# Performance work log

Hardware: AMD Instinct MI355X
Metric: run time of the kernel (lower is better)

Reference implementation:

```python
import jax, jax.numpy as jnp
import numpy as np


def gcn_conv(x, W, b, src, dst, num_nodes):
    """PyG GCNConv with add_self_loops=True, symmetric normalization, bias.
    src/dst already include self-loops. deg computed from unit edge weights."""
    deg = jax.ops.segment_sum(jnp.ones(src.shape[0], x.dtype), dst,
                              num_segments=num_nodes)
    dinv = jnp.where(deg > 0, jax.lax.rsqrt(deg), 0.0)
    norm = dinv[src] * dinv[dst]               # [E]
    h = x @ W                                  # [N, F_out] dense GEMM first
    msg = h[src] * norm[:, None]               # gather + scale, [E, F_out]
    out = jax.ops.segment_sum(msg, dst, num_segments=num_nodes)  # scatter-add
    return out + b


def setup_inputs() -> dict:
    key = jax.random.key(0)
    ks = jax.random.split(key, 5)
    N, E, F_in, F_out = 50000, 800000, 512, 40
    x = jax.random.normal(ks[0], (N, F_in), dtype=jnp.float32)
    edge_index = jax.random.randint(ks[1], (2, E), 0, N, dtype=jnp.int64)
    W1 = jax.random.normal(ks[2], (F_in, 256), dtype=jnp.float32) * (F_in ** -0.5)
    W2 = jax.random.normal(ks[3], (256, 16), dtype=jnp.float32) * (256 ** -0.5)
    W3 = jax.random.normal(ks[4], (16, F_out), dtype=jnp.float32) * (16 ** -0.5)
    return {
        "x": x, "edge_index": edge_index,
        "W1": W1, "b1": jnp.zeros((256,), jnp.float32),
        "W2": W2, "b2": jnp.zeros((16,), jnp.float32),
        "W3": W3, "b3": jnp.zeros((F_out,), jnp.float32),
    }


def reference(x, edge_index, W1, b1, W2, b2, W3, b3):
    N = x.shape[0]
    loop = jnp.arange(N, dtype=edge_index.dtype)
    src = jnp.concatenate([edge_index[0], loop])  # self-loops appended once,
    dst = jnp.concatenate([edge_index[1], loop])  # shared by all three layers
    h = gcn_conv(x, W1, b1, src, dst, N)
    h = jax.nn.relu(h)                 # dropout is identity in eval mode
    h = gcn_conv(h, W2, b2, src, dst, N)
    h = jax.nn.relu(h)
    h = gcn_conv(h, W3, b3, src, dst, N)
    return jax.nn.log_softmax(h, axis=1)
```

## Files before the change

kernel.cpp:

```cpp
#include <hip/hip_runtime.h>
#include <hip/hip_bf16.h>
#include <math.h>

typedef __hip_bfloat16 bf16;
typedef __attribute__((ext_vector_type(8))) __bf16 bf16x8;
typedef __attribute__((ext_vector_type(4))) float f32x4;

#define KIN 512
#define F1  256
#define F2  16
#define F3  40
#define NBIN 64


__device__ inline unsigned pk_bf2(float a, float b) {
  bf16 x = __float2bfloat16(a), y = __float2bfloat16(b);
  unsigned short ux = *(unsigned short*)&x, uy = *(unsigned short*)&y;
  return (unsigned)ux | ((unsigned)uy << 16);
}
__device__ inline float bfbits(unsigned u16) {
  unsigned v = u16 << 16;
  return *(float*)&v;
}
__device__ inline void async16(const void* g, void* l) {
  __builtin_amdgcn_global_load_lds((const __attribute__((address_space(1))) void*)g,
                                   (__attribute__((address_space(3))) void*)l, 16, 0, 0);
}
__device__ inline void accum8(float* acc, uint4 h, float w) {
  acc[0] = fmaf(w, bfbits(h.x & 0xffff), acc[0]);
  acc[1] = fmaf(w, bfbits(h.x >> 16),    acc[1]);
  acc[2] = fmaf(w, bfbits(h.y & 0xffff), acc[2]);
  acc[3] = fmaf(w, bfbits(h.y >> 16),    acc[3]);
  acc[4] = fmaf(w, bfbits(h.z & 0xffff), acc[4]);
  acc[5] = fmaf(w, bfbits(h.z >> 16),    acc[5]);
  acc[6] = fmaf(w, bfbits(h.w & 0xffff), acc[6]);
  acc[7] = fmaf(w, bfbits(h.w >> 16),    acc[7]);
}


__global__ __launch_bounds__(256) void k_init2(int* __restrict__ cnt,
                                               const int* __restrict__ ei, int* __restrict__ flag,
                                               const float* __restrict__ W,
                                               unsigned short* __restrict__ Wt,
                                               int* __restrict__ hist,
                                               int n, int nb) {
  int b = blockIdx.x;
  int t = threadIdx.x;
  if (b < nb) {
    int i = b * 256 + t;
    if (i < n) cnt[i] = 0;
    if (b == 0 && t < NBIN) hist[t] = 0;
    if (b == 0 && t == 0)
      *flag = (ei[1] == 0 && ei[3] == 0 && ei[5] == 0 && ei[7] == 0) ? 1 : 0;
  } else {
    __shared__ float tile[32][33];
    int b2 = b - nb;
    int k0 = (b2 & 15) * 32;
    int n0 = (b2 >> 4) * 32;
    int lr = t >> 5, lc = t & 31;
#pragma unroll
    for (int rr = 0; rr < 32; rr += 8)
      tile[lr + rr][lc] = W[(size_t)(k0 + lr + rr) * F1 + n0 + lc];
    __syncthreads();
#pragma unroll
    for (int rr = 0; rr < 32; rr += 8) {
      bf16 v = __float2bfloat16(tile[lc][lr + rr]);
      Wt[(size_t)(n0 + lr + rr) * KIN + k0 + lc] = *(unsigned short*)&v;
    }
  }
}


__global__ __launch_bounds__(256) void k_count_conv(const int* __restrict__ ei,
                                                    const int* __restrict__ flag,
                                                    int* __restrict__ cnt,
                                                    int* __restrict__ rank,
                                                    int E, int nct, int stride,
                                                    const float* __restrict__ X,
                                                    unsigned short* __restrict__ Xb,
                                                    int total8) {
  int b = blockIdx.x;
  int t = threadIdx.x;
  bool is_cnt = (b % stride == 0) && (b / stride < nct);
  if (is_cnt) {
    int e = (b / stride) * 256 + t;
    if (e >= E) return;
    int is64 = *flag;
    int d = is64 ? ei[2 * E + 2 * e] : ei[E + e];
    rank[e] = atomicAdd(&cnt[d], 1);
  } else {
    int nb_before = (b + stride - 1) / stride;
    if (nb_before > nct) nb_before = nct;
    int idx = (b - nb_before) * 256 + t;
    if (idx >= total8) return;
    const float4* src = (const float4*)X + (size_t)idx * 2;
    float4 f0 = src[0], f1 = src[1];
    uint4 pk;
    pk.x = pk_bf2(f0.x, f0.y); pk.y = pk_bf2(f0.z, f0.w);
    pk.z = pk_bf2(f1.x, f1.y); pk.w = pk_bf2(f1.z, f1.w);
    ((uint4*)Xb)[idx] = pk;
  }
}

__global__ __launch_bounds__(256) void k_scan1(const int* __restrict__ cnt,
                                               int* __restrict__ off,
                                               int* __restrict__ bsum,
                                               float* __restrict__ dinv,
                                               int* __restrict__ hist, int N) {
  __shared__ int s[256];
  __shared__ int lh[NBIN];
  int t = threadIdx.x;
  if (t < NBIN) lh[t] = 0;
  int base = blockIdx.x * 1024 + t * 4;
  int v0 = (base + 0 < N) ? cnt[base + 0] : 0;
  int v1 = (base + 1 < N) ? cnt[base + 1] : 0;
  int v2 = (base + 2 < N) ? cnt[base + 2] : 0;
  int v3 = (base + 3 < N) ? cnt[base + 3] : 0;
  if (base + 0 < N) dinv[base + 0] = rsqrtf((float)(v0 + 1));
  if (base + 1 < N) dinv[base + 1] = rsqrtf((float)(v1 + 1));
  if (base + 2 < N) dinv[base + 2] = rsqrtf((float)(v2 + 1));
  if (base + 3 < N) dinv[base + 3] = rsqrtf((float)(v3 + 1));
  int tsum = v0 + v1 + v2 + v3;
  s[t] = tsum;
  __syncthreads();
  if (base + 0 < N) atomicAdd(&lh[v0 < 63 ? v0 : 63], 1);
  if (base + 1 < N) atomicAdd(&lh[v1 < 63 ? v1 : 63], 1);
  if (base + 2 < N) atomicAdd(&lh[v2 < 63 ? v2 : 63], 1);
  if (base + 3 < N) atomicAdd(&lh[v3 < 63 ? v3 : 63], 1);
  for (int d = 1; d < 256; d <<= 1) {
    int u = (t >= d) ? s[t - d] : 0;
    __syncthreads();
    s[t] += u;
    __syncthreads();
  }
  int excl = s[t] - tsum;
  int p0 = excl + v0, p1 = p0 + v1, p2 = p1 + v2, p3 = p2 + v3;
  if (base + 0 < N) off[base + 1] = p0;
  if (base + 1 < N) off[base + 2] = p1;
  if (base + 2 < N) off[base + 3] = p2;
  if (base + 3 < N) off[base + 4] = p3;
  if (t == 255) bsum[blockIdx.x] = s[255];
  if (t < NBIN) {
    int h = lh[t];
    if (h) atomicAdd(&hist[t], h);
  }
}

__global__ __launch_bounds__(256) void k_scan3m(int* __restrict__ off,
                                                const int* __restrict__ bsum,
                                                const int* __restrict__ hist,
                                                int* __restrict__ binoff, int N) {
  __shared__ int cs;
  int t = threadIdx.x;
  if (t < 64) {
    int v = (t < blockIdx.x) ? bsum[t] : 0;
    for (int d = 32; d; d >>= 1) v += __shfl_xor(v, d, 64);
    if (t == 0) cs = v;
  }
  if (blockIdx.x == 0 && t < NBIN) {
    int a = 0;
    for (int j = 0; j < t; ++j) a += hist[j];
    binoff[t] = a;
  }
  __syncthreads();
  int c = cs;
  int base = blockIdx.x * 1024 + t * 4;
#pragma unroll
  for (int k = 0; k < 4; ++k)
    if (base + k < N) off[base + k + 1] += c;
  if (blockIdx.x == 0 && t == 0) off[0] = 0;
}


__global__ __launch_bounds__(256) void k_gemm1_sc(const unsigned short* __restrict__ Ab,
                                                  const unsigned short* __restrict__ Bt,
                                                  bf16* __restrict__ C, int M, int ngx,
                                                  const int* __restrict__ ei,
                                                  const int* __restrict__ flag,
                                                  const int* __restrict__ off,
                                                  const int* __restrict__ rank,
                                                  const float* __restrict__ dinv,
                                                  int2* __restrict__ ew, int E, int ebk,
                                                  const int* __restrict__ cnt,
                                                  int* __restrict__ binoff,
                                                  int* __restrict__ perm) {
  __shared__ unsigned short As[128 * 32];
  __shared__ unsigned short Bs[128 * 32];
  __shared__ int lh[NBIN], lb[NBIN];
  int b = blockIdx.x;
  int t = threadIdx.x;
  int ngemm = ngx * 2;
  if (b >= ngemm + ebk) {
    int idx = (b - ngemm - ebk) * 256 + t;
    if (t < NBIN) lh[t] = 0;
    __syncthreads();
    int bin = 0, lr2 = 0;
    bool valid = (idx < M);
    if (valid) {
      int d = cnt[idx];
      bin = d < 63 ? d : 63;
      lr2 = atomicAdd(&lh[bin], 1);
    }
    __syncthreads();
    if (t < NBIN && lh[t] > 0) lb[t] = atomicAdd(&binoff[t], lh[t]);
    __syncthreads();
    if (valid) perm[lb[bin] + lr2] = idx;
    return;
  }
  if (b >= ngemm) {
    int e = (b - ngemm) * 256 + t;
    if (e >= E) return;
    int is64 = *flag;
    int s, d;
    if (is64) { s = ei[2 * e]; d = ei[2 * E + 2 * e]; }
    else      { s = ei[e];     d = ei[E + e]; }
    int pos = off[d] + rank[e];
    float w = dinv[s] * dinv[d];
    ew[pos] = make_int2(s, __float_as_int(w));
    return;
  }
  int wave = t >> 6, lane = t & 63;
  int wm = wave >> 1, wn = wave & 1;
  int row0 = (b % ngx) * 128, col0 = (b / ngx) * 128;
  int q = lane >> 4, m16 = lane & 15;
  int srow = lane >> 2, schk = lane & 3;

  f32x4 acc[4][4];
#pragma unroll
  for (int i = 0; i < 4; ++i)
#pragma unroll
    for (int j = 0; j < 4; ++j) acc[i][j] = {0.f, 0.f, 0.f, 0.f};

  for (int kb = 0; kb < 16; ++kb) {
    __syncthreads();
#pragma unroll
    for (int jj = 0; jj < 2; ++jj) {
      int lr = wave * 32 + jj * 16 + srow;
      int gr = row0 + lr; if (gr >= M) gr = M - 1;
      int gchk = schk ^ ((lr >> 1) & 3);
      async16(Ab + (size_t)gr * KIN + kb * 32 + gchk * 8,
              As + (wave * 32 + jj * 16) * 32);
    }
#pragma unroll
    for (int jj = 0; jj < 2; ++jj) {
      int lr = wave * 32 + jj * 16 + srow;
      int gchk = schk ^ ((lr >> 1) & 3);
      async16(Bt + (size_t)(col0 + lr) * KIN + kb * 32 + gchk * 8,
              Bs + (wave * 32 + jj * 16) * 32);
    }
    __syncthreads();
    bf16x8 af[4], bfr[4];
#pragma unroll
    for (int i = 0; i < 4; ++i) {
      int m = wm * 64 + i * 16 + m16;
      af[i] = *(const bf16x8*)(As + m * 32 + ((q ^ ((m >> 1) & 3)) * 8));
    }
#pragma unroll
    for (int j = 0; j < 4; ++j) {
      int n = wn * 64 + j * 16 + m16;
      bfr[j] = *(const bf16x8*)(Bs + n * 32 + ((q ^ ((n >> 1) & 3)) * 8));
    }
#pragma unroll
    for (int j = 0; j < 4; ++j)
#pragma unroll
      for (int i = 0; i < 4; ++i)
        acc[i][j] = __builtin_amdgcn_mfma_f32_16x16x32_bf16(af[i], bfr[j], acc[i][j], 0, 0, 0);
  }

#pragma unroll
  for (int i = 0; i < 4; ++i) {
#pragma unroll
    for (int r = 0; r < 4; ++r) {
      int row = row0 + wm * 64 + i * 16 + q * 4 + r;
      if (row < M) {
#pragma unroll
        for (int j = 0; j < 4; ++j) {
          int col = col0 + wn * 64 + j * 16 + m16;
          C[(size_t)row * F1 + col] = __float2bfloat16(acc[i][j][r]);
        }
      }
    }
  }
}


__global__ __launch_bounds__(256) void k_agg1(const bf16* __restrict__ H,
                                              const int* __restrict__ off,
                                              const int2* __restrict__ ew,
                                              const float* __restrict__ dinv,
                                              const float* __restrict__ bias,
                                              const int* __restrict__ perm,
                                              bf16* __restrict__ O, int N, int nbb) {
  int b = blockIdx.x;
  int t = threadIdx.x;
  int phase = (b >= nbb) ? 1 : 0;
  int b2 = b - phase * nbb;
  int idx = b2 * 16 + (t >> 4);
  if (idx >= N) return;
  int i = perm[idx];
  int f0 = phase * 128 + (t & 15) * 8;
  const unsigned short* Hu = (const unsigned short*)H;
  float di = dinv[i];
  float w0 = di * di;
  float acc[8];
  {
    uint4 h = *(const uint4*)(Hu + (size_t)i * F1 + f0);
    acc[0] = w0 * bfbits(h.x & 0xffff); acc[1] = w0 * bfbits(h.x >> 16);
    acc[2] = w0 * bfbits(h.y & 0xffff); acc[3] = w0 * bfbits(h.y >> 16);
    acc[4] = w0 * bfbits(h.z & 0xffff); acc[5] = w0 * bfbits(h.z >> 16);
    acc[6] = w0 * bfbits(h.w & 0xffff); acc[7] = w0 * bfbits(h.w >> 16);
  }
  int e = off[i], e1 = off[i + 1];
  for (; e + 8 <= e1; e += 8) {
    int2 p0 = ew[e + 0], p1 = ew[e + 1], p2 = ew[e + 2], p3 = ew[e + 3];
    int2 p4 = ew[e + 4], p5 = ew[e + 5], p6 = ew[e + 6], p7 = ew[e + 7];
    uint4 g0 = *(const uint4*)(Hu + (size_t)p0.x * F1 + f0);
    uint4 g1 = *(const uint4*)(Hu + (size_t)p1.x * F1 + f0);
    uint4 g2 = *(const uint4*)(Hu + (size_t)p2.x * F1 + f0);
    uint4 g3 = *(const uint4*)(Hu + (size_t)p3.x * F1 + f0);
    uint4 g4 = *(const uint4*)(Hu + (size_t)p4.x * F1 + f0);
    uint4 g5 = *(const uint4*)(Hu + (size_t)p5.x * F1 + f0);
    uint4 g6 = *(const uint4*)(Hu + (size_t)p6.x * F1 + f0);
    uint4 g7 = *(const uint4*)(Hu + (size_t)p7.x * F1 + f0);
    accum8(acc, g0, __int_as_float(p0.y));
    accum8(acc, g1, __int_as_float(p1.y));
    accum8(acc, g2, __int_as_float(p2.y));
    accum8(acc, g3, __int_as_float(p3.y));
    accum8(acc, g4, __int_as_float(p4.y));
    accum8(acc, g5, __int_as_float(p5.y));
    accum8(acc, g6, __int_as_float(p6.y));
    accum8(acc, g7, __int_as_float(p7.y));
  }
  for (; e < e1; ++e) {
    int2 pe = ew[e];
    uint4 g = *(const uint4*)(Hu + (size_t)pe.x * F1 + f0);
    accum8(acc, g, __int_as_float(pe.y));
  }
  float4 b0 = *(const float4*)(bias + f0);
  float4 b1 = *(const float4*)(bias + f0 + 4);
  float bb[8] = {b0.x, b0.y, b0.z, b0.w, b1.x, b1.y, b1.z, b1.w};
  uint4 o;
  unsigned* op = (unsigned*)&o;
#pragma unroll
  for (int k = 0; k < 4; ++k) {
    float lo = fmaxf(acc[2 * k] + bb[2 * k], 0.f);
    float hi = fmaxf(acc[2 * k + 1] + bb[2 * k + 1], 0.f);
    op[k] = pk_bf2(lo, hi);
  }
  *(uint4*)((unsigned short*)O + (size_t)i * F1 + f0) = o;
}


__global__ __launch_bounds__(256) void k_gemm2(const bf16* __restrict__ A,
                                               const float* __restrict__ W,
                                               float* __restrict__ C, int N) {
  __shared__ float Ws[F1 * F2];
  __shared__ float Ts[16][F1];
  int t = threadIdx.x;
  int r0 = blockIdx.x * 16;
#pragma unroll
  for (int j = 0; j < 16; ++j) Ws[t + 256 * j] = W[t + 256 * j];
  const unsigned short* Au = (const unsigned short*)A;
#pragma unroll
  for (int j = 0; j < 2; ++j) {
    int idx = t + 256 * j;
    int r = idx >> 5;
    int c8 = (idx & 31) * 8;
    int row = r0 + r;
    uint4 g = make_uint4(0, 0, 0, 0);
    if (row < N) g = *(const uint4*)(Au + (size_t)row * F1 + c8);
    float* ts = &Ts[r][c8];
    ts[0] = bfbits(g.x & 0xffff); ts[1] = bfbits(g.x >> 16);
    ts[2] = bfbits(g.y & 0xffff); ts[3] = bfbits(g.y >> 16);
    ts[4] = bfbits(g.z & 0xffff); ts[5] = bfbits(g.z >> 16);
    ts[6] = bfbits(g.w & 0xffff); ts[7] = bfbits(g.w >> 16);
  }
  __syncthreads();
  int r = t >> 4, c = t & 15;
  float acc = 0.f;
  const float4* tv = (const float4*)&Ts[r][0];
#pragma unroll 8
  for (int k4 = 0; k4 < 64; ++k4) {
    float4 a = tv[k4];
    int k = k4 * 4;
    acc = fmaf(a.x, Ws[(k + 0) * 16 + c], acc);
    acc = fmaf(a.y, Ws[(k + 1) * 16 + c], acc);
    acc = fmaf(a.z, Ws[(k + 2) * 16 + c], acc);
    acc = fmaf(a.w, Ws[(k + 3) * 16 + c], acc);
  }
  int row = r0 + r;
  if (row < N) C[(size_t)row * F2 + c] = acc;
}


__global__ __launch_bounds__(256) void k_agg16(const float* __restrict__ H,
                                               const int* __restrict__ off,
                                               const int2* __restrict__ ew,
                                               const float* __restrict__ dinv,
                                               const float* __restrict__ bias,
                                               const int* __restrict__ perm,
                                               float* __restrict__ O, int N) {
  int t = threadIdx.x;
  int idx = blockIdx.x * 16 + (t >> 4);
  int f = t & 15;
  if (idx >= N) return;
  int i = perm[idx];
  float di = dinv[i];
  float acc = di * di * H[(size_t)i * F2 + f];
  int e = off[i], e1 = off[i + 1];
  for (; e + 4 <= e1; e += 4) {
    int2 p0 = ew[e + 0], p1 = ew[e + 1], p2 = ew[e + 2], p3 = ew[e + 3];
    float g0 = H[(size_t)p0.x * F2 + f];
    float g1 = H[(size_t)p1.x * F2 + f];
    float g2 = H[(size_t)p2.x * F2 + f];
    float g3 = H[(size_t)p3.x * F2 + f];
    acc = fmaf(__int_as_float(p0.y), g0, acc);
    acc = fmaf(__int_as_float(p1.y), g1, acc);
    acc = fmaf(__int_as_float(p2.y), g2, acc);
    acc = fmaf(__int_as_float(p3.y), g3, acc);
  }
  for (; e < e1; ++e) {
    int2 pe = ew[e];
    acc = fmaf(__int_as_float(pe.y), H[(size_t)pe.x * F2 + f], acc);
  }
  acc = fmaxf(acc + bias[f], 0.f);
  O[(size_t)i * F2 + f] = acc;
}


__global__ __launch_bounds__(256) void k_agg3_g3(const float* __restrict__ H,
                                                 const int* __restrict__ off,
                                                 const int2* __restrict__ ew,
                                                 const float* __restrict__ dinv,
                                                 const float* __restrict__ W3,
                                                 const float* __restrict__ b3,
                                                 const int* __restrict__ perm,
                                                 float* __restrict__ O, int N) {
  __shared__ float W3s[F2 * F3];
  __shared__ float b3s[F3];
  __shared__ float aggs[16 * 17];
  int t = threadIdx.x;
  for (int idx2 = t; idx2 < F2 * F3; idx2 += 256) W3s[idx2] = W3[idx2];
  if (t < F3) b3s[t] = b3[t];
  __syncthreads();

  int node = t >> 4, f = t & 15;
  int idx = blockIdx.x * 16 + node;
  if (idx >= N) return;
  int i = perm[idx];
  float di = dinv[i];
  float acc = di * di * H[(size_t)i * F2 + f];
  int e = off[i], e1 = off[i + 1];
  for (; e + 4 <= e1; e += 4) {
    int2 p0 = ew[e + 0], p1 = ew[e + 1], p2 = ew[e + 2], p3 = ew[e + 3];
    float g0 = H[(size_t)p0.x * F2 + f];
    float g1 = H[(size_t)p1.x * F2 + f];
    float g2 = H[(size_t)p2.x * F2 + f];
    float g3 = H[(size_t)p3.x * F2 + f];
    acc = fmaf(__int_as_float(p0.y), g0, acc);
    acc = fmaf(__int_as_float(p1.y), g1, acc);
    acc = fmaf(__int_as_float(p2.y), g2, acc);
    acc = fmaf(__int_as_float(p3.y), g3, acc);
  }
  for (; e < e1; ++e) {
    int2 pe = ew[e];
    acc = fmaf(__int_as_float(pe.y), H[(size_t)pe.x * F2 + f], acc);
  }
  aggs[node * 17 + f] = acc;

  const float* ar = &aggs[node * 17];
  float o0 = b3s[f], o1 = b3s[f + 16], o2 = (f < 8) ? b3s[f + 32] : 0.f;
#pragma unroll
  for (int k = 0; k < F2; ++k) {
    float a = ar[k];
    o0 = fmaf(a, W3s[k * F3 + f], o0);
    o1 = fmaf(a, W3s[k * F3 + f + 16], o1);
    if (f < 8) o2 = fmaf(a, W3s[k * F3 + f + 32], o2);
  }
  float m = fmaxf(o0, o1);
  if (f < 8) m = fmaxf(m, o2);
#pragma unroll
  for (int d = 1; d < 16; d <<= 1) m = fmaxf(m, __shfl_xor(m, d, 16));
  float s = __expf(o0 - m) + __expf(o1 - m) + ((f < 8) ? __expf(o2 - m) : 0.f);
#pragma unroll
  for (int d = 1; d < 16; d <<= 1) s += __shfl_xor(s, d, 16);
  float lse = m + __logf(s);
  float* orow = O + (size_t)i * F3;
  orow[f] = o0 - lse;
  orow[f + 16] = o1 - lse;
  if (f < 8) orow[f + 32] = o2 - lse;
}


extern "C" void kernel_launch(void* const* d_in, const int* in_sizes, int n_in,
                              void* d_out, int out_size, void* d_ws, size_t ws_size,
                              hipStream_t stream) {
  const float* x  = (const float*)d_in[0];
  const int*   ei = (const int*)d_in[1];
  const float* W1 = (const float*)d_in[2];
  const float* b1 = (const float*)d_in[3];
  const float* W2 = (const float*)d_in[4];
  const float* b2 = (const float*)d_in[5];
  const float* W3 = (const float*)d_in[6];
  const float* b3 = (const float*)d_in[7];
  float* out = (float*)d_out;

  int N = in_sizes[0] / KIN;
  int E = in_sizes[1] / 2;

  char* p = (char*)d_ws;
  auto take = [&](size_t bytes) {
    char* r = p;
    p += (bytes + 255) & ~(size_t)255;
    return r;
  };
  int*   flag  = (int*)take(4);
  int*   cnt   = (int*)take((size_t)N * 4);
  int*   off   = (int*)take((size_t)(N + 1) * 4);
  float* dinv  = (float*)take((size_t)N * 4);
  int*   bsum  = (int*)take(64 * 4);
  int*   hist  = (int*)take(NBIN * 4);
  int*   binoff= (int*)take(NBIN * 4);
  int*   perm  = (int*)take((size_t)N * 4);
  int*   rank  = (int*)take((size_t)E * 4);
  int2*  ew    = (int2*)take((size_t)E * 8);
  unsigned short* w1t = (unsigned short*)take((size_t)KIN * F1 * 2);
  unsigned short* xb  = (unsigned short*)take((size_t)N * KIN * 2);
  bf16*  h1    = (bf16*)take((size_t)N * F1 * 2);
  bf16*  out1  = (bf16*)take((size_t)N * F1 * 2);
  float* h2    = (float*)take((size_t)N * F2 * 4);
  float* out2  = (float*)take((size_t)N * F2 * 4);

  int nb  = (N + 255) / 256;
  int ebk = (E + 255) / 256;
  int nsc = (N + 1023) / 1024;
  int total8 = (N * KIN) / 8;
  int cvb = (total8 + 255) / 256;
  int tot = ebk + cvb;
  int stride = tot / ebk; if (stride < 1) stride = 1;

  k_init2<<<nb + 128, 256, 0, stream>>>(cnt, ei, flag, W1, w1t, hist, N, nb);
  k_count_conv<<<tot, 256, 0, stream>>>(ei, flag, cnt, rank, E, ebk, stride, x, xb, total8);
  k_scan1<<<nsc, 256, 0, stream>>>(cnt, off, bsum, dinv, hist, N);
  k_scan3m<<<nsc, 256, 0, stream>>>(off, bsum, hist, binoff, N);

  int ngx = (N + 127) / 128;
  k_gemm1_sc<<<ngx * 2 + ebk + nb, 256, 0, stream>>>(xb, w1t, h1, N, ngx,
                                                     ei, flag, off, rank, dinv, ew, E, ebk,
                                                     cnt, binoff, perm);

  int nbb = (N + 15) / 16;
  k_agg1<<<nbb * 2, 256, 0, stream>>>(h1, off, ew, dinv, b1, perm, out1, N, nbb);
  k_gemm2<<<(N + 15) / 16, 256, 0, stream>>>(out1, W2, h2, N);
  k_agg16<<<(N + 15) / 16, 256, 0, stream>>>(h2, off, ew, dinv, b2, perm, out2, N);
  k_agg3_g3<<<(N + 15) / 16, 256, 0, stream>>>(out2, off, ew, dinv, W3, b3, perm, out, N);
}
```

Baseline: 348.3 us.

## Fuse layer-1 aggregation with layer-2 GEMM and reverse degree-bin order

Merges the layer-1 neighbor aggregation (bias+ReLU) with the 256x16 layer-2 GEMM. Aggregated rows stay in shared memory instead of being written to and re-read from a bf16 intermediate buffer. Each block now covers 8 nodes with 32 threads per node over all 256 features, replacing the two feature-half phases. Bin offsets are computed in reverse, so perm appears to put high-degree bins first to reduce tail imbalance. The cost is that each block reloads 16KB of W2 into LDS and uses only half its threads for the GEMM.

```diff
diff --git a/kernel.cpp b/kernel.cpp
--- a/kernel.cpp
+++ b/kernel.cpp
@@ -11,6 +11,7 @@
 #define F2  16
 #define F3  40
 #define NBIN 64
+#define TSS 264
 
 
 __device__ inline unsigned pk_bf2(float a, float b) {
@@ -159,7 +160,7 @@
   }
   if (blockIdx.x == 0 && t < NBIN) {
     int a = 0;
-    for (int j = 0; j < t; ++j) a += hist[j];
+    for (int j = t + 1; j < NBIN; ++j) a += hist[j];
     binoff[t] = a;
   }
   __syncthreads();
@@ -284,21 +285,23 @@
 }
 
 
-__global__ __launch_bounds__(256) void k_agg1(const bf16* __restrict__ H,
-                                              const int* __restrict__ off,
-                                              const int2* __restrict__ ew,
-                                              const float* __restrict__ dinv,
-                                              const float* __restrict__ bias,
-                                              const int* __restrict__ perm,
-                                              bf16* __restrict__ O, int N, int nbb) {
-  int b = blockIdx.x;
-  int t = threadIdx.x;
-  int phase = (b >= nbb) ? 1 : 0;
-  int b2 = b - phase * nbb;
-  int idx = b2 * 16 + (t >> 4);
-  if (idx >= N) return;
-  int i = perm[idx];
-  int f0 = phase * 128 + (t & 15) * 8;
+__global__ __launch_bounds__(256) void k_agg1g2(const bf16* __restrict__ H,
+                                                const int* __restrict__ off,
+                                                const int2* __restrict__ ew,
+                                                const float* __restrict__ dinv,
+                                                const float* __restrict__ b1,
+                                                const int* __restrict__ perm,
+                                                const float* __restrict__ W2,
+                                                float* __restrict__ h2, int N) {
+  __shared__ float W2s[F1 * F2];
+  __shared__ float Ts[8][TSS];
+  int t = threadIdx.x;
+#pragma unroll
+  for (int j = 0; j < 16; ++j) W2s[t + 256 * j] = W2[t + 256 * j];
+  int idx = blockIdx.x * 8 + (t >> 5);
+  int cidx = idx < N ? idx : N - 1;
+  int i = perm[cidx];
+  int f0 = (t & 31) * 8;
   const unsigned short* Hu = (const unsigned short*)H;
   float di = dinv[i];
   float w0 = di * di;
@@ -336,60 +339,35 @@
     uint4 g = *(const uint4*)(Hu + (size_t)pe.x * F1 + f0);
     accum8(acc, g, __int_as_float(pe.y));
   }
-  float4 b0 = *(const float4*)(bias + f0);
-  float4 b1 = *(const float4*)(bias + f0 + 4);
-  float bb[8] = {b0.x, b0.y, b0.z, b0.w, b1.x, b1.y, b1.z, b1.w};
-  uint4 o;
-  unsigned* op = (unsigned*)&o;
-#pragma unroll
-  for (int k = 0; k < 4; ++k) {
-    float lo = fmaxf(acc[2 * k] + bb[2 * k], 0.f);
-    float hi = fmaxf(acc[2 * k + 1] + bb[2 * k + 1], 0.f);
-    op[k] = pk_bf2(lo, hi);
-  }
-  *(uint4*)((unsigned short*)O + (size_t)i * F1 + f0) = o;
-}
-
-
-__global__ __launch_bounds__(256) void k_gemm2(const bf16* __restrict__ A,
-                                               const float* __restrict__ W,
-                                               float* __restrict__ C, int N) {
-  __shared__ float Ws[F1 * F2];
-  __shared__ float Ts[16][F1];
-  int t = threadIdx.x;
-  int r0 = blockIdx.x * 16;
-#pragma unroll
-  for (int j = 0; j < 16; ++j) Ws[t + 256 * j] = W[t + 256 * j];
-  const unsigned short* Au = (const unsigned short*)A;
-#pragma unroll
-  for (int j = 0; j < 2; ++j) {
-    int idx = t + 256 * j;
-    int r = idx >> 5;
-    int c8 = (idx & 31) * 8;
-    int row = r0 + r;
-    uint4 g = make_uint4(0, 0, 0, 0);
-    if (row < N) g = *(const uint4*)(Au + (size_t)row * F1 + c8);
-    float* ts = &Ts[r][c8];
-    ts[0] = bfbits(g.x & 0xffff); ts[1] = bfbits(g.x >> 16);
-    ts[2] = bfbits(g.y & 0xffff); ts[3] = bfbits(g.y >> 16);
-    ts[4] = bfbits(g.z & 0xffff); ts[5] = bfbits(g.z >> 16);
-    ts[6] = bfbits(g.w & 0xffff); ts[7] = bfbits(g.w >> 16);
-  }
+  float4 bb0 = *(const float4*)(b1 + f0);
+  float4 bb1 = *(const float4*)(b1 + f0 + 4);
+  int node = t >> 5;
+  float* ts = &Ts[node][f0];
+  ts[0] = fmaxf(acc[0] + bb0.x, 0.f);
+  ts[1] = fmaxf(acc[1] + bb0.y, 0.f);
+  ts[2] = fmaxf(acc[2] + bb0.z, 0.f);
+  ts[3] = fmaxf(acc[3] + bb0.w, 0.f);
+  ts[4] = fmaxf(acc[4] + bb1.x, 0.f);
+  ts[5] = fmaxf(acc[5] + bb1.y, 0.f);
+  ts[6] = fmaxf(acc[6] + bb1.z, 0.f);
+  ts[7] = fmaxf(acc[7] + bb1.w, 0.f);
   __syncthreads();
-  int r = t >> 4, c = t & 15;
-  float acc = 0.f;
-  const float4* tv = (const float4*)&Ts[r][0];
+  if (t < 128) {
+    int n2 = t >> 4, c = t & 15;
+    int gi = blockIdx.x * 8 + n2;
+    float s = 0.f;
+    const float4* tv = (const float4*)&Ts[n2][0];
 #pragma unroll 8
-  for (int k4 = 0; k4 < 64; ++k4) {
-    float4 a = tv[k4];
-    int k = k4 * 4;
-    acc = fmaf(a.x, Ws[(k + 0) * 16 + c], acc);
-    acc = fmaf(a.y, Ws[(k + 1) * 16 + c], acc);
-    acc = fmaf(a.z, Ws[(k + 2) * 16 + c], acc);
-    acc = fmaf(a.w, Ws[(k + 3) * 16 + c], acc);
-  }
-  int row = r0 + r;
-  if (row < N) C[(size_t)row * F2 + c] = acc;
+    for (int k4 = 0; k4 < 64; ++k4) {
+      float4 a = tv[k4];
+      int k = k4 * 4;
+      s = fmaf(a.x, W2s[(k + 0) * 16 + c], s);
+      s = fmaf(a.y, W2s[(k + 1) * 16 + c], s);
+      s = fmaf(a.z, W2s[(k + 2) * 16 + c], s);
+      s = fmaf(a.w, W2s[(k + 3) * 16 + c], s);
+    }
+    if (gi < N) h2[(size_t)perm[gi] * F2 + c] = s;
+  }
 }
 
 
@@ -527,7 +505,6 @@
   unsigned short* w1t = (unsigned short*)take((size_t)KIN * F1 * 2);
   unsigned short* xb  = (unsigned short*)take((size_t)N * KIN * 2);
   bf16*  h1    = (bf16*)take((size_t)N * F1 * 2);
-  bf16*  out1  = (bf16*)take((size_t)N * F1 * 2);
   float* h2    = (float*)take((size_t)N * F2 * 4);
   float* out2  = (float*)take((size_t)N * F2 * 4);
 
@@ -549,9 +526,7 @@
                                                      ei, flag, off, rank, dinv, ew, E, ebk,
                                                      cnt, binoff, perm);
 
-  int nbb = (N + 15) / 16;
-  k_agg1<<<nbb * 2, 256, 0, stream>>>(h1, off, ew, dinv, b1, perm, out1, N, nbb);
-  k_gemm2<<<(N + 15) / 16, 256, 0, stream>>>(out1, W2, h2, N);
+  k_agg1g2<<<(N + 7) / 8, 256, 0, stream>>>(h1, off, ew, dinv, b1, perm, W2, h2, N);
   k_agg16<<<(N + 15) / 16, 256, 0, stream>>>(h2, off, ew, dinv, b2, perm, out2, N);
   k_agg3_g3<<<(N + 15) / 16, 256, 0, stream>>>(out2, off, ew, dinv, W3, b3, perm, out, N);
 }
```

Result: faster. 322.7 us (-7.4%).
